# Kernel optimization log

Measured on AMD Instinct MI355X. Metric: run time of the kernel, lower is better.

The kernel has to match this reference:

```python
import jax, jax.numpy as jnp
import numpy as np
from itertools import product

D = 96  # input grid resolution; after subdivision it is 2*D = 192
N_VOX = 20000
C_IN = 64
C_OUT = 64

OFFSETS = jnp.array(list(product([-1, 0, 1], repeat=3)), dtype=jnp.int32)   # [27,3] conv neighborhood
CHILD = jnp.array(list(product([0, 1], repeat=3)), dtype=jnp.int32)        # [8,3] subdivision children


def _lin(coords, d):
    # linearize (z,y,x)-style coords into a flat index for the dense lookup grid
    return (coords[:, 0] * d + coords[:, 1]) * d + coords[:, 2]


def _submanifold_conv3d(coords, feats, W, b, d):
    """Submanifold sparse 3x3x3 conv: output only at active sites.
    coords: [N,3] int32, feats: [N,Cin], W: [27,Cin,Cout], b: [Cout]."""
    n = coords.shape[0]
    grid = jnp.full((d * d * d,), -1, dtype=jnp.int32).at[_lin(coords, d)].set(
        jnp.arange(n, dtype=jnp.int32))
    out = jnp.broadcast_to(b, (n, b.shape[0])).astype(feats.dtype)
    for k in range(27):  # fixed small kernel loop (unrolled under jit)
        nb = coords + OFFSETS[k]
        inb = jnp.all((nb >= 0) & (nb < d), axis=1)
        idx = grid[_lin(jnp.clip(nb, 0, d - 1), d)]
        mask = (inb & (idx >= 0)).astype(feats.dtype)
        f = feats[jnp.maximum(idx, 0)] * mask[:, None]  # gather active neighbors
        out = out + f @ W[k]
    return out


def setup_inputs() -> dict:
    rng = np.random.default_rng(0)
    lin = rng.choice(D ** 3, size=N_VOX, replace=False)  # unique active voxels
    coords = np.stack([lin // (D * D), (lin // D) % D, lin % D], axis=1).astype(np.int32)
    key = jax.random.key(0)
    k1, k2, k3, k4, k5 = jax.random.split(key, 5)
    scale = 1.0 / np.sqrt(27.0 * C_IN)
    return {
        "coords": jnp.asarray(coords),
        "feats": jax.random.normal(k1, (N_VOX, C_IN), jnp.float32),
        "W1": jax.random.normal(k2, (27, C_IN, C_OUT), jnp.float32) * scale,
        "b1": jax.random.normal(k3, (C_OUT,), jnp.float32) * 0.01,
        "W2": jax.random.normal(k4, (27, C_OUT, C_OUT), jnp.float32) * scale,
        "b2": jax.random.normal(k5, (C_OUT,), jnp.float32) * 0.01,
    }


def reference(coords, feats, W1, b1, W2, b2):
    # act_layers: SparseConv3d + SiLU
    h = jax.nn.silu(_submanifold_conv3d(coords, feats, W1, b1, D))
    n = coords.shape[0]
    coords2 = ((coords * 2)[:, None, :] + CHILD[None, :, :]).reshape(8 * n, 3)
    h2 = jnp.repeat(h, 8, axis=0)  # matches (N,8,C)->(8N,C) child order
    # out_layers: SparseConv3d + SiLU at doubled resolution
    return jax.nn.silu(_submanifold_conv3d(coords2, h2, W2, b2, 2 * D))
```

## Files before the change

### kernel.cpp

```cpp
#include <hip/hip_runtime.h>

#define D1 96
#define GRID_VOX (D1 * D1 * D1)
#define CAP1 32
#define CAP2S 8

typedef __attribute__((ext_vector_type(8))) short short8_t;
typedef __attribute__((ext_vector_type(4))) float f32x4;

__device__ __forceinline__ unsigned short bf16rne(float x) {
    unsigned u = __float_as_uint(x);
    return (unsigned short)((u + 0x7FFF + ((u >> 16) & 1)) >> 16);
}
__device__ __forceinline__ void split2(float v, unsigned short& hi,
                                       unsigned short& lo) {
    hi = bf16rne(v);
    float hf = __uint_as_float((unsigned)hi << 16);
    lo = bf16rne(v - hf);
}

__global__ void setup_kernel(const float* __restrict__ W1,
                             const float* __restrict__ W2,
                             int4* __restrict__ grid16,
                             unsigned short* __restrict__ Wpk1h,
                             unsigned short* __restrict__ Wpk1l,
                             unsigned short* __restrict__ Wpk2h,
                             unsigned short* __restrict__ Wpk2l,
                             float* __restrict__ W2e) {
    int b = blockIdx.x;
    if (b < 432) {
        grid16[b * 256 + threadIdx.x] = make_int4(0, 0, 0, 0);
        return;
    }
    int t = (b - 432) * 256 + threadIdx.x;
    if (t < 512) {
        int fid = t >> 6, l = t & 63;
        int kb = fid >> 2, c = fid & 3;
#pragma unroll
        for (int e = 0; e < 8; ++e) {
            int ci = kb * 32 + ((l >> 4) << 3) + e;
            int co = c * 16 + (l & 15);
            unsigned short hi, lo;
            split2(W1[13 * 4096 + ci * 64 + co], hi, lo);
            Wpk1h[(size_t)t * 8 + e] = hi;
            Wpk1l[(size_t)t * 8 + e] = lo;
        }
    } else if (t < 512 + 4096) {
        int u = t - 512;
        int fid = u >> 6, l = u & 63;
        int s = fid >> 3, kb = (fid >> 2) & 1, c = fid & 3;
        int s0 = (s >> 2) & 1, s1 = (s >> 1) & 1, s2 = s & 1;
#pragma unroll
        for (int e = 0; e < 8; ++e) {
            int ci = kb * 32 + ((l >> 4) << 3) + e;
            int co = c * 16 + (l & 15);
            float sum = 0.f;
            for (int o0 = -s0; o0 <= 1 - s0; ++o0)
                for (int o1 = -s1; o1 <= 1 - s1; ++o1)
                    for (int o2 = -s2; o2 <= 1 - s2; ++o2) {
                        int k = (o0 + 1) * 9 + (o1 + 1) * 3 + (o2 + 1);
                        sum += W2[k * 4096 + ci * 64 + co];
                    }
            unsigned short hi, lo;
            split2(sum, hi, lo);
            Wpk2h[(size_t)u * 8 + e] = hi;
            Wpk2l[(size_t)u * 8 + e] = lo;
        }
    } else {
        int r = t - 4608;
        if (r >= 64 * 4096) return;
        int sd = r >> 12, e = r & 4095;
        int s = sd >> 3, d = sd & 7;
        int sa[3] = { (s >> 2) & 1, (s >> 1) & 1, s & 1 };
        int da[3] = { (d >> 2) & 1, (d >> 1) & 1, d & 1 };
        int lo_[3], hi_[3];
        for (int a = 0; a < 3; ++a) {
            int p = sa[a] - 1 + da[a];
            int l = 2 * p - sa[a];     if (l < -1) l = -1;
            int h = 2 * p + 1 - sa[a]; if (h > 1) h = 1;
            lo_[a] = l; hi_[a] = h;
        }
        float sum = 0.f;
        for (int o0 = lo_[0]; o0 <= hi_[0]; ++o0)
            for (int o1 = lo_[1]; o1 <= hi_[1]; ++o1)
                for (int o2 = lo_[2]; o2 <= hi_[2]; ++o2) {
                    int k = (o0 + 1) * 9 + (o1 + 1) * 3 + (o2 + 1);
                    sum += W2[k * 4096 + e];
                }
        W2e[(size_t)sd * 4096 + e] = sum;
    }
}

__global__ void scatter_grid_kernel(const int* __restrict__ coords,
                                    unsigned short* __restrict__ grid, int n) {
    int i = blockIdx.x * blockDim.x + threadIdx.x;
    if (i < n)
        grid[(coords[3 * i] * D1 + coords[3 * i + 1]) * D1 + coords[3 * i + 2]] =
            (unsigned short)(i + 1);
}

__global__ void build_pairs_kernel(const int* __restrict__ coords,
                                   const unsigned short* __restrict__ grid,
                                   int* __restrict__ c1, int* __restrict__ p1,
                                   int* __restrict__ c2s, int* __restrict__ p2s,
                                   int n) {
    int i = blockIdx.x * blockDim.x + threadIdx.x;
    if (i >= n) return;
    int c0 = coords[3 * i], cc1 = coords[3 * i + 1], cc2 = coords[3 * i + 2];

    int jv[27];
#pragma unroll
    for (int k = 0; k < 27; ++k) {
        int o0 = k / 9 - 1, o1 = (k / 3) % 3 - 1, o2 = k % 3 - 1;
        int x0 = c0 + o0, x1 = cc1 + o1, x2 = cc2 + o2;
        bool inb = (unsigned)x0 < D1 && (unsigned)x1 < D1 && (unsigned)x2 < D1;
        jv[k] = inb ? (int)grid[(x0 * D1 + x1) * D1 + x2] - 1 : -1;
    }

    int n1 = 0;
    int n2[8] = {0, 0, 0, 0, 0, 0, 0, 0};
#pragma unroll
    for (int k = 0; k < 27; ++k) {
        if (k == 13) continue;
        int j = jv[k];
        if (j < 0) continue;
        int o0 = k / 9 - 1, o1 = (k / 3) % 3 - 1, o2 = k % 3 - 1;
        p1[(size_t)i * CAP1 + n1] = j | (k << 17);
        ++n1;
#pragma unroll
        for (int s = 0; s < 8; ++s) {
            int d0 = o0 + 1 - ((s >> 2) & 1);
            int d1 = o1 + 1 - ((s >> 1) & 1);
            int d2 = o2 + 1 - (s & 1);
            if (((d0 | d1 | d2) & ~1) == 0) {
                int d = (d0 << 2) | (d1 << 1) | d2;
                p2s[((size_t)i * 8 + s) * CAP2S + n2[s]] = j | (d << 17);
                ++n2[s];
            }
        }
    }
    c1[i] = n1;
#pragma unroll
    for (int s = 0; s < 8; ++s) c2s[i * 8 + s] = n2[s];
}

__device__ __forceinline__ void load_split_A(const float* __restrict__ src,
                                             int arow, int lane, short8_t& ah0,
                                             short8_t& al0, short8_t& ah1,
                                             short8_t& al1) {
    const float* ap = src + (size_t)arow * 64 + ((lane >> 4) << 3);
    f32x4 a0 = *(const f32x4*)(ap);
    f32x4 a1 = *(const f32x4*)(ap + 4);
    f32x4 a2 = *(const f32x4*)(ap + 32);
    f32x4 a3 = *(const f32x4*)(ap + 36);
#pragma unroll
    for (int e = 0; e < 4; ++e) {
        unsigned short hh, ll;
        split2(a0[e], hh, ll); ah0[e] = (short)hh; al0[e] = (short)ll;
        split2(a1[e], hh, ll); ah0[4 + e] = (short)hh; al0[4 + e] = (short)ll;
        split2(a2[e], hh, ll); ah1[e] = (short)hh; al1[e] = (short)ll;
        split2(a3[e], hh, ll); ah1[4 + e] = (short)hh; al1[4 + e] = (short)ll;
    }
}

__device__ __forceinline__ void dense_mfma(const short8_t ah0, const short8_t al0,
                                           const short8_t ah1, const short8_t al1,
                                           const short8_t* __restrict__ Bh,
                                           const short8_t* __restrict__ Bl,
                                           const float* __restrict__ bias,
                                           float* __restrict__ oT, int w,
                                           int lane) {
#pragma unroll 1
    for (int c = 0; c < 4; ++c) {
        short8_t bh0 = Bh[c * 64 + lane];
        short8_t bl0 = Bl[c * 64 + lane];
        short8_t bh1 = Bh[(4 + c) * 64 + lane];
        short8_t bl1 = Bl[(4 + c) * 64 + lane];
        f32x4 acc = {0.f, 0.f, 0.f, 0.f};
        acc = __builtin_amdgcn_mfma_f32_16x16x32_bf16(ah0, bh0, acc, 0, 0, 0);
        acc = __builtin_amdgcn_mfma_f32_16x16x32_bf16(al0, bh0, acc, 0, 0, 0);
        acc = __builtin_amdgcn_mfma_f32_16x16x32_bf16(ah0, bl0, acc, 0, 0, 0);
        acc = __builtin_amdgcn_mfma_f32_16x16x32_bf16(ah1, bh1, acc, 0, 0, 0);
        acc = __builtin_amdgcn_mfma_f32_16x16x32_bf16(al1, bh1, acc, 0, 0, 0);
        acc = __builtin_amdgcn_mfma_f32_16x16x32_bf16(ah1, bl1, acc, 0, 0, 0);
        int col = c * 16 + (lane & 15);
        float bb = bias[col];
#pragma unroll
        for (int r = 0; r < 4; ++r) {
            int row = w * 16 + ((lane >> 4) << 2) + r;
            oT[row * 64 + col] = acc[r] + bb;
        }
    }
}

__device__ __forceinline__ void fixup_pair_lds(const float* __restrict__ fj,
                                               const float* __restrict__ wk,
                                               float* __restrict__ oT, int row,
                                               int lane) {
    float a0 = 0.f, a1 = 0.f, a2 = 0.f, a3 = 0.f;
#pragma unroll
    for (int c4 = 0; c4 < 16; ++c4) {
        f32x4 fv = *(const f32x4*)(fj + c4 * 4);
        a0 += fv[0] * wk[(c4 * 4 + 0) * 64 + lane];
        a1 += fv[1] * wk[(c4 * 4 + 1) * 64 + lane];
        a2 += fv[2] * wk[(c4 * 4 + 2) * 64 + lane];
        a3 += fv[3] * wk[(c4 * 4 + 3) * 64 + lane];
    }
    atomicAdd(&oT[row * 64 + lane], (a0 + a1) + (a2 + a3));
}

__device__ __forceinline__ void scan64(int cnt, int lane, int* pfxs, int* cnts,
                                       int* nps) {
    int val = cnt;
#pragma unroll
    for (int off = 1; off < 64; off <<= 1) {
        int v2 = __shfl_up(val, off);
        if (lane >= off) val += v2;
    }
    pfxs[lane] = val - cnt;
    cnts[lane] = cnt;
    if (lane == 63) nps[0] = val;
}

__global__ __launch_bounds__(256) void conv1_fused_kernel(
    const float* __restrict__ feats, const float* __restrict__ W1,
    const unsigned short* __restrict__ Wpk1h,
    const unsigned short* __restrict__ Wpk1l, const float* __restrict__ b1,
    const int* __restrict__ c1, const int* __restrict__ p1,
    float* __restrict__ h, int n) {
    __shared__ __align__(16) float oT[4096];
    __shared__ __align__(16) float fstage[64 * 64];
    __shared__ int pl[2048];
    __shared__ int pfxs[64], cnts_s[64], nps[1];
    int base = blockIdx.x * 64;
    int t = threadIdx.x, w = t >> 6, lane = t & 63;

    if (t < 64) {
        int cnt = (base + lane < n) ? c1[base + lane] : 0;
        scan64(cnt, lane, pfxs, cnts_s, nps);
    }

    int arow = base + w * 16 + (lane & 15);
    if (arow >= n) arow = n - 1;
    short8_t ah0, al0, ah1, al1;
    load_split_A(feats, arow, lane, ah0, al0, ah1, al1);
    dense_mfma(ah0, al0, ah1, al1, (const short8_t*)Wpk1h,
               (const short8_t*)Wpk1l, b1, oT, w, lane);
    __syncthreads();

    {
        int row = t & 63, e0 = t >> 6;
        int cr = cnts_s[row], pf = pfxs[row];
        for (int e = e0; e < cr; e += 4)
            pl[pf + e] = p1[(size_t)(base + row) * CAP1 + e] | (row << 23);
    }
    __syncthreads();

    int np = nps[0];
    for (int cb = 0; cb < np; cb += 64) {
        {
            int p = cb + (t >> 2), qq = t & 3;
            if (p < np) {
                int j = pl[p] & 0x1FFFF;
                const f32x4* src = (const f32x4*)(feats + (size_t)j * 64 + qq * 16);
                f32x4* dst = (f32x4*)&fstage[(p - cb) * 64 + qq * 16];
#pragma unroll
                for (int q = 0; q < 4; ++q) dst[q] = src[q];
            }
        }
        __syncthreads();
        int pe = np < cb + 64 ? np : cb + 64;
#pragma unroll 1
        for (int p = cb + w; p < pe; p += 4) {
            int se = pl[p];
            int k = (se >> 17) & 31, row = (se >> 23) & 63;
            fixup_pair_lds(&fstage[(p - cb) * 64], W1 + (size_t)k * 4096, oT,
                           row, lane);
        }
        __syncthreads();
    }

    {
        int r = t >> 2, q0 = (t & 3) * 16;
        if (base + r < n) {
#pragma unroll
            for (int jj = 0; jj < 4; ++jj) {
                f32x4 v = *(f32x4*)&oT[r * 64 + q0 + jj * 4];
#pragma unroll
                for (int u = 0; u < 4; ++u) v[u] = v[u] / (1.f + __expf(-v[u]));
                *(f32x4*)&h[(size_t)(base + r) * 64 + q0 + jj * 4] = v;
            }
        }
    }
}

__global__ __launch_bounds__(256) void conv2_fused_kernel(
    const float* __restrict__ h, const unsigned short* __restrict__ Wpk2h,
    const unsigned short* __restrict__ Wpk2l, const float* __restrict__ W2e,
    const float* __restrict__ b2, const int* __restrict__ c2s,
    const int* __restrict__ p2s, float* __restrict__ out, int n) {
    __shared__ __align__(16) float oT[4096];
    __shared__ __align__(16) float fstage[32 * 64];
    __shared__ int pl[512];
    __shared__ int pfxs[64], cnts_s[64], nps[1];
    int base = blockIdx.x * 64, s = blockIdx.y;
    int t = threadIdx.x, w = t >> 6, lane = t & 63;

    if (t < 64) {
        int cnt = (base + lane < n) ? c2s[(size_t)(base + lane) * 8 + s] : 0;
        scan64(cnt, lane, pfxs, cnts_s, nps);
    }

    int arow = base + w * 16 + (lane & 15);
    if (arow >= n) arow = n - 1;
    short8_t ah0, al0, ah1, al1;
    load_split_A(h, arow, lane, ah0, al0, ah1, al1);
    dense_mfma(ah0, al0, ah1, al1,
               (const short8_t*)Wpk2h + (size_t)s * 8 * 64,
               (const short8_t*)Wpk2l + (size_t)s * 8 * 64, b2, oT, w, lane);
    __syncthreads();

    {
        int row = t & 63, e0 = t >> 6;
        int cr = cnts_s[row], pf = pfxs[row];
        for (int e = e0; e < cr; e += 4)
            pl[pf + e] =
                p2s[((size_t)(base + row) * 8 + s) * CAP2S + e] | (row << 23);
    }
    __syncthreads();

    int np = nps[0];
    for (int cb = 0; cb < np; cb += 32) {
        {
            int p = cb + (t >> 3), qq = t & 7;
            if (p < np) {
                int j = pl[p] & 0x1FFFF;
                const f32x4* src = (const f32x4*)(h + (size_t)j * 64 + qq * 8);
                f32x4* dst = (f32x4*)&fstage[(p - cb) * 64 + qq * 8];
                dst[0] = src[0];
                dst[1] = src[1];
            }
        }
        __syncthreads();
        int pe = np < cb + 32 ? np : cb + 32;
#pragma unroll 1
        for (int p = cb + w; p < pe; p += 4) {
            int se = pl[p];
            int d = (se >> 17) & 31, row = (se >> 23) & 63;
            fixup_pair_lds(&fstage[(p - cb) * 64],
                           W2e + (size_t)(s * 8 + d) * 4096, oT, row, lane);
        }
        __syncthreads();
    }

    {
        int r = t >> 2, q0 = (t & 3) * 16;
        if (base + r < n) {
#pragma unroll
            for (int jj = 0; jj < 4; ++jj) {
                f32x4 v = *(f32x4*)&oT[r * 64 + q0 + jj * 4];
#pragma unroll
                for (int u = 0; u < 4; ++u) v[u] = v[u] / (1.f + __expf(-v[u]));
                *(f32x4*)&out[((size_t)(base + r) * 8 + s) * 64 + q0 + jj * 4] = v;
            }
        }
    }
}

extern "C" void kernel_launch(void* const* d_in, const int* in_sizes, int n_in,
                              void* d_out, int out_size, void* d_ws,
                              size_t ws_size, hipStream_t stream) {
    const int* coords = (const int*)d_in[0];
    const float* feats = (const float*)d_in[1];
    const float* W1 = (const float*)d_in[2];
    const float* b1 = (const float*)d_in[3];
    const float* W2 = (const float*)d_in[4];
    const float* b2 = (const float*)d_in[5];
    float* out = (float*)d_out;

    int n = in_sizes[0] / 3;
    int nblk = (n + 63) / 64;

    char* ws = (char*)d_ws;
    size_t off = 0;
    auto alloc = [&](size_t bytes) {
        size_t o = off;
        off = (off + bytes + 255) & ~(size_t)255;
        return o;
    };
    unsigned short* grid1 = (unsigned short*)(ws + alloc((size_t)GRID_VOX * 2));
    float* h      = (float*)(ws + alloc((size_t)n * 64 * 4));
    float* W2e    = (float*)(ws + alloc(64 * 4096 * 4));
    unsigned short* Wpk1h = (unsigned short*)(ws + alloc(512 * 8 * 2));
    unsigned short* Wpk1l = (unsigned short*)(ws + alloc(512 * 8 * 2));
    unsigned short* Wpk2h = (unsigned short*)(ws + alloc(4096 * 8 * 2));
    unsigned short* Wpk2l = (unsigned short*)(ws + alloc(4096 * 8 * 2));
    int*   c1     = (int*)(ws + alloc((size_t)n * 9 * 4));
    int*   c2s    = c1 + n;
    int*   p1     = (int*)(ws + alloc((size_t)n * CAP1 * 4));
    int*   p2s    = (int*)(ws + alloc((size_t)n * 8 * CAP2S * 4));

    setup_kernel<<<1474, 256, 0, stream>>>(W1, W2, (int4*)grid1, Wpk1h, Wpk1l,
                                           Wpk2h, Wpk2l, W2e);
    scatter_grid_kernel<<<(n + 255) / 256, 256, 0, stream>>>(coords, grid1, n);
    build_pairs_kernel<<<(n + 255) / 256, 256, 0, stream>>>(
        coords, grid1, c1, p1, c2s, p2s, n);

    conv1_fused_kernel<<<nblk, 256, 0, stream>>>(feats, W1, Wpk1h, Wpk1l, b1,
                                                 c1, p1, h, n);
    conv2_fused_kernel<<<dim3(nblk, 8), 256, 0, stream>>>(
        h, Wpk2h, Wpk2l, W2e, b2, c2s, p2s, out, n);
}
```

Baseline: 88.18 us.

## Split conv2 into sparse fixup kernel and dense MFMA kernel

Replaces the fused conv2 kernel (one block per 64 rows per subdivision child, with LDS staging of neighbor pairs) with two kernels. A per-voxel wave kernel first computes cross-parent neighbor contributions directly into out, skipping voxels with no pairs. A 512-thread dense MFMA kernel then handles all 8 children per block with the A fragments shared in LDS, adding bias, any fixup partial and SiLU. This removes the redundant per-s reloading of h and the LDS pair staging, at the cost of an extra launch and a read-modify-write of out.

```diff
diff --git a/kernel.cpp b/kernel.cpp
--- a/kernel.cpp
+++ b/kernel.cpp
@@ -17,6 +17,9 @@
     hi = bf16rne(v);
     float hf = __uint_as_float((unsigned)hi << 16);
     lo = bf16rne(v - hf);
+}
+__device__ __forceinline__ float silu(float v) {
+    return v / (1.f + __expf(-v));
 }
 
 __global__ void setup_kernel(const float* __restrict__ W1,
@@ -287,81 +290,136 @@
             for (int jj = 0; jj < 4; ++jj) {
                 f32x4 v = *(f32x4*)&oT[r * 64 + q0 + jj * 4];
 #pragma unroll
-                for (int u = 0; u < 4; ++u) v[u] = v[u] / (1.f + __expf(-v[u]));
+                for (int u = 0; u < 4; ++u) v[u] = silu(v[u]);
                 *(f32x4*)&h[(size_t)(base + r) * 64 + q0 + jj * 4] = v;
             }
         }
     }
 }
 
-__global__ __launch_bounds__(256) void conv2_fused_kernel(
+__global__ __launch_bounds__(256) void conv2_fix_kernel(
+    const float* __restrict__ h, const float* __restrict__ W2e,
+    const int* __restrict__ c2s, const int* __restrict__ p2s,
+    float* __restrict__ out, int n) {
+    int w = threadIdx.x >> 6, lane = threadIdx.x & 63;
+    int i = blockIdx.x * 4 + w;
+    if (i >= n) return;
+    int cnt8 = (lane < 8) ? c2s[(size_t)i * 8 + lane] : 0;
+    if (__ballot(cnt8 > 0) == 0ULL) return;
+
+#pragma unroll 1
+    for (int s = 0; s < 8; ++s) {
+        int cl = __shfl(cnt8, s);
+        if (cl == 0) continue;
+        float tot = 0.f;
+#pragma unroll 1
+        for (int e = 0; e < cl; ++e) {
+            int se = __builtin_amdgcn_readfirstlane(
+                p2s[((size_t)i * 8 + s) * CAP2S + e]);
+            int j = se & 0x1FFFF, d = (se >> 17) & 7;
+            const float* fj = h + (size_t)j * 64;
+            const float* wk = W2e + (size_t)(s * 8 + d) * 4096;
+            float a0 = 0.f, a1 = 0.f, a2 = 0.f, a3 = 0.f;
+#pragma unroll
+            for (int c4 = 0; c4 < 16; ++c4) {
+                f32x4 fv = *(const f32x4*)(fj + c4 * 4);
+                a0 += fv[0] * wk[(c4 * 4 + 0) * 64 + lane];
+                a1 += fv[1] * wk[(c4 * 4 + 1) * 64 + lane];
+                a2 += fv[2] * wk[(c4 * 4 + 2) * 64 + lane];
+                a3 += fv[3] * wk[(c4 * 4 + 3) * 64 + lane];
+            }
+            tot += (a0 + a1) + (a2 + a3);
+        }
+        out[((size_t)i * 8 + s) * 64 + lane] = tot;
+    }
+}
+
+__global__ __launch_bounds__(512) void conv2_dense_kernel(
     const float* __restrict__ h, const unsigned short* __restrict__ Wpk2h,
-    const unsigned short* __restrict__ Wpk2l, const float* __restrict__ W2e,
-    const float* __restrict__ b2, const int* __restrict__ c2s,
-    const int* __restrict__ p2s, float* __restrict__ out, int n) {
-    __shared__ __align__(16) float oT[4096];
-    __shared__ __align__(16) float fstage[32 * 64];
-    __shared__ int pl[512];
-    __shared__ int pfxs[64], cnts_s[64], nps[1];
-    int base = blockIdx.x * 64, s = blockIdx.y;
-    int t = threadIdx.x, w = t >> 6, lane = t & 63;
-
-    if (t < 64) {
-        int cnt = (base + lane < n) ? c2s[(size_t)(base + lane) * 8 + s] : 0;
-        scan64(cnt, lane, pfxs, cnts_s, nps);
-    }
-
-    int arow = base + w * 16 + (lane & 15);
-    if (arow >= n) arow = n - 1;
-    short8_t ah0, al0, ah1, al1;
-    load_split_A(h, arow, lane, ah0, al0, ah1, al1);
-    dense_mfma(ah0, al0, ah1, al1,
-               (const short8_t*)Wpk2h + (size_t)s * 8 * 64,
-               (const short8_t*)Wpk2l + (size_t)s * 8 * 64, b2, oT, w, lane);
+    const unsigned short* __restrict__ Wpk2l, const float* __restrict__ b2,
+    const int* __restrict__ c2s, float* __restrict__ out, int n) {
+    __shared__ short8_t afrag[2][4][2][64];
+    int base = blockIdx.x * 64;
+    int t = threadIdx.x, lane = t & 63, u = t >> 6;
+
+    {
+        int tr = u >> 1, kb = u & 1;
+        int gr = base + tr * 16 + (lane & 15);
+        if (gr >= n) gr = n - 1;
+        const float* ap = h + (size_t)gr * 64 + kb * 32 + ((lane >> 4) << 3);
+        f32x4 a0 = *(const f32x4*)ap;
+        f32x4 a1 = *(const f32x4*)(ap + 4);
+        short8_t hi, lo;
+#pragma unroll
+        for (int e = 0; e < 4; ++e) {
+            unsigned short hh, ll;
+            split2(a0[e], hh, ll); hi[e] = (short)hh; lo[e] = (short)ll;
+            split2(a1[e], hh, ll); hi[4 + e] = (short)hh; lo[4 + e] = (short)ll;
+        }
+        afrag[0][tr][kb][lane] = hi;
+        afrag[1][tr][kb][lane] = lo;
+    }
     __syncthreads();
 
-    {
-        int row = t & 63, e0 = t >> 6;
-        int cr = cnts_s[row], pf = pfxs[row];
-        for (int e = e0; e < cr; e += 4)
-            pl[pf + e] =
-                p2s[((size_t)(base + row) * 8 + s) * CAP2S + e] | (row << 23);
-    }
-    __syncthreads();
-
-    int np = nps[0];
-    for (int cb = 0; cb < np; cb += 32) {
-        {
-            int p = cb + (t >> 3), qq = t & 7;
-            if (p < np) {
-                int j = pl[p] & 0x1FFFF;
-                const f32x4* src = (const f32x4*)(h + (size_t)j * 64 + qq * 8);
-                f32x4* dst = (f32x4*)&fstage[(p - cb) * 64 + qq * 8];
-                dst[0] = src[0];
-                dst[1] = src[1];
-            }
-        }
-        __syncthreads();
-        int pe = np < cb + 32 ? np : cb + 32;
-#pragma unroll 1
-        for (int p = cb + w; p < pe; p += 4) {
-            int se = pl[p];
-            int d = (se >> 17) & 31, row = (se >> 23) & 63;
-            fixup_pair_lds(&fstage[(p - cb) * 64],
-                           W2e + (size_t)(s * 8 + d) * 4096, oT, row, lane);
-        }
-        __syncthreads();
-    }
-
-    {
-        int r = t >> 2, q0 = (t & 3) * 16;
-        if (base + r < n) {
-#pragma unroll
-            for (int jj = 0; jj < 4; ++jj) {
-                f32x4 v = *(f32x4*)&oT[r * 64 + q0 + jj * 4];
-#pragma unroll
-                for (int u = 0; u < 4; ++u) v[u] = v[u] / (1.f + __expf(-v[u]));
-                *(f32x4*)&out[((size_t)(base + r) * 8 + s) * 64 + q0 + jj * 4] = v;
+    int s = u;
+    int ci = base + lane; if (ci >= n) ci = n - 1;
+    bool flag = (base + lane < n) && (c2s[(size_t)ci * 8 + s] > 0);
+    unsigned long long pmask = __ballot(flag);
+
+    const short8_t* Bh = (const short8_t*)Wpk2h;
+    const short8_t* Bl = (const short8_t*)Wpk2l;
+    short8_t bh[4][2], bl[4][2];
+#pragma unroll
+    for (int tc = 0; tc < 4; ++tc)
+#pragma unroll
+        for (int kb = 0; kb < 2; ++kb) {
+            bh[tc][kb] = Bh[(size_t)(((s * 2 + kb) * 4 + tc)) * 64 + lane];
+            bl[tc][kb] = Bl[(size_t)(((s * 2 + kb) * 4 + tc)) * 64 + lane];
+        }
+
+    f32x4 acc[4][4];
+#pragma unroll
+    for (int a = 0; a < 4; ++a)
+#pragma unroll
+        for (int b = 0; b < 4; ++b) acc[a][b] = (f32x4){0.f, 0.f, 0.f, 0.f};
+
+#pragma unroll
+    for (int tr = 0; tr < 4; ++tr) {
+        short8_t ah0 = afrag[0][tr][0][lane];
+        short8_t al0 = afrag[1][tr][0][lane];
+        short8_t ah1 = afrag[0][tr][1][lane];
+        short8_t al1 = afrag[1][tr][1][lane];
+#pragma unroll
+        for (int tc = 0; tc < 4; ++tc) {
+            f32x4 a = acc[tr][tc];
+            a = __builtin_amdgcn_mfma_f32_16x16x32_bf16(ah0, bh[tc][0], a, 0, 0, 0);
+            a = __builtin_amdgcn_mfma_f32_16x16x32_bf16(al0, bh[tc][0], a, 0, 0, 0);
+            a = __builtin_amdgcn_mfma_f32_16x16x32_bf16(ah0, bl[tc][0], a, 0, 0, 0);
+            a = __builtin_amdgcn_mfma_f32_16x16x32_bf16(ah1, bh[tc][1], a, 0, 0, 0);
+            a = __builtin_amdgcn_mfma_f32_16x16x32_bf16(al1, bh[tc][1], a, 0, 0, 0);
+            a = __builtin_amdgcn_mfma_f32_16x16x32_bf16(ah1, bl[tc][1], a, 0, 0, 0);
+            acc[tr][tc] = a;
+        }
+    }
+
+    float bb[4];
+#pragma unroll
+    for (int tc = 0; tc < 4; ++tc) bb[tc] = b2[tc * 16 + (lane & 15)];
+
+#pragma unroll
+    for (int tr = 0; tr < 4; ++tr) {
+#pragma unroll
+        for (int r4 = 0; r4 < 4; ++r4) {
+            int R = tr * 16 + ((lane >> 4) << 2) + r4;
+            bool valid = (base + R) < n;
+            bool hasp = valid && ((pmask >> R) & 1ULL);
+            size_t orow = ((size_t)(base + R) * 8 + s) * 64;
+#pragma unroll
+            for (int tc = 0; tc < 4; ++tc) {
+                float v = acc[tr][tc][r4] + bb[tc];
+                if (hasp) v += out[orow + tc * 16 + (lane & 15)];
+                v = silu(v);
+                if (valid) out[orow + tc * 16 + (lane & 15)] = v;
             }
         }
     }
@@ -408,6 +466,7 @@
 
     conv1_fused_kernel<<<nblk, 256, 0, stream>>>(feats, W1, Wpk1h, Wpk1l, b1,
                                                  c1, p1, h, n);
-    conv2_fused_kernel<<<dim3(nblk, 8), 256, 0, stream>>>(
-        h, Wpk2h, Wpk2l, W2e, b2, c2s, p2s, out, n);
-}
+    conv2_fix_kernel<<<(n + 3) / 4, 256, 0, stream>>>(h, W2e, c2s, p2s, out, n);
+    conv2_dense_kernel<<<nblk, 512, 0, stream>>>(h, Wpk2h, Wpk2l, b2, c2s, out,
+                                                 n);
+}
```

Measured after the change: 107.1 us. +21.4%, slower.

## Bin neighbor pairs by kernel offset and keep weight slice in registers

Applied to the files above, without the earlier changes.

Sorts each block's neighbor pair list into bins by kernel offset with an LDS counting sort. Each wave then handles whole bins, loading the 64-entry weight column for that offset into registers once. Neighbor features are read straight from global memory, one float per lane with the next one prefetched, and broadcast by shuffle, which replaces LDS staging of features and per-pair weight reads from global. The risks are load imbalance across the 4 waves, since bins are assigned round-robin, extra register pressure from the 64 weights, and smaller pair-list capacity (1664 and 448 instead of 2048 and 512).

```diff
diff --git a/kernel.cpp b/kernel.cpp
--- a/kernel.cpp
+++ b/kernel.cpp
@@ -17,6 +17,9 @@
     hi = bf16rne(v);
     float hf = __uint_as_float((unsigned)hi << 16);
     lo = bf16rne(v - hf);
+}
+__device__ __forceinline__ float silu(float v) {
+    return v / (1.f + __expf(-v));
 }
 
 __global__ void setup_kernel(const float* __restrict__ W1,
@@ -193,22 +196,6 @@
     }
 }
 
-__device__ __forceinline__ void fixup_pair_lds(const float* __restrict__ fj,
-                                               const float* __restrict__ wk,
-                                               float* __restrict__ oT, int row,
-                                               int lane) {
-    float a0 = 0.f, a1 = 0.f, a2 = 0.f, a3 = 0.f;
-#pragma unroll
-    for (int c4 = 0; c4 < 16; ++c4) {
-        f32x4 fv = *(const f32x4*)(fj + c4 * 4);
-        a0 += fv[0] * wk[(c4 * 4 + 0) * 64 + lane];
-        a1 += fv[1] * wk[(c4 * 4 + 1) * 64 + lane];
-        a2 += fv[2] * wk[(c4 * 4 + 2) * 64 + lane];
-        a3 += fv[3] * wk[(c4 * 4 + 3) * 64 + lane];
-    }
-    atomicAdd(&oT[row * 64 + lane], (a0 + a1) + (a2 + a3));
-}
-
 __device__ __forceinline__ void scan64(int cnt, int lane, int* pfxs, int* cnts,
                                        int* nps) {
     int val = cnt;
@@ -220,6 +207,40 @@
     pfxs[lane] = val - cnt;
     cnts[lane] = cnt;
     if (lane == 63) nps[0] = val;
+}
+
+__device__ __forceinline__ void bin_fixups(const float* __restrict__ src,
+                                           const float* __restrict__ wk,
+                                           const int* __restrict__ pls, int s0,
+                                           int s1, float* __restrict__ oT,
+                                           int lane) {
+    float wreg[64];
+#pragma unroll
+    for (int ci = 0; ci < 64; ++ci) wreg[ci] = wk[ci * 64 + lane];
+
+    int e = pls[s0];
+    float fv = src[(size_t)(e & 0x1FFFF) * 64 + lane];
+#pragma unroll 1
+    for (int p = s0; p < s1; ++p) {
+        int en = 0;
+        float fvn = 0.f;
+        if (p + 1 < s1) {
+            en = pls[p + 1];
+            fvn = src[(size_t)(en & 0x1FFFF) * 64 + lane];
+        }
+        int row = (e >> 23) & 63;
+        float a0 = 0.f, a1 = 0.f, a2 = 0.f, a3 = 0.f;
+#pragma unroll
+        for (int ci = 0; ci < 64; ci += 4) {
+            a0 += __shfl(fv, ci + 0) * wreg[ci + 0];
+            a1 += __shfl(fv, ci + 1) * wreg[ci + 1];
+            a2 += __shfl(fv, ci + 2) * wreg[ci + 2];
+            a3 += __shfl(fv, ci + 3) * wreg[ci + 3];
+        }
+        atomicAdd(&oT[row * 64 + lane], (a0 + a1) + (a2 + a3));
+        e = en;
+        fv = fvn;
+    }
 }
 
 __global__ __launch_bounds__(256) void conv1_fused_kernel(
@@ -229,9 +250,9 @@
     const int* __restrict__ c1, const int* __restrict__ p1,
     float* __restrict__ h, int n) {
     __shared__ __align__(16) float oT[4096];
-    __shared__ __align__(16) float fstage[64 * 64];
-    __shared__ int pl[2048];
+    __shared__ int pl[1664], pls[1664];
     __shared__ int pfxs[64], cnts_s[64], nps[1];
+    __shared__ int binStart[29], binCur[28];
     int base = blockIdx.x * 64;
     int t = threadIdx.x, w = t >> 6, lane = t & 63;
 
@@ -239,6 +260,7 @@
         int cnt = (base + lane < n) ? c1[base + lane] : 0;
         scan64(cnt, lane, pfxs, cnts_s, nps);
     }
+    if (t >= 64 && t < 92) binCur[t - 64] = 0;
 
     int arow = base + w * 16 + (lane & 15);
     if (arow >= n) arow = n - 1;
@@ -257,28 +279,33 @@
     __syncthreads();
 
     int np = nps[0];
-    for (int cb = 0; cb < np; cb += 64) {
-        {
-            int p = cb + (t >> 2), qq = t & 3;
-            if (p < np) {
-                int j = pl[p] & 0x1FFFF;
-                const f32x4* src = (const f32x4*)(feats + (size_t)j * 64 + qq * 16);
-                f32x4* dst = (f32x4*)&fstage[(p - cb) * 64 + qq * 16];
-#pragma unroll
-                for (int q = 0; q < 4; ++q) dst[q] = src[q];
-            }
-        }
-        __syncthreads();
-        int pe = np < cb + 64 ? np : cb + 64;
+    for (int p = t; p < np; p += 256) atomicAdd(&binCur[(pl[p] >> 17) & 31], 1);
+    __syncthreads();
+    if (t == 0) {
+        int acc = 0;
+        for (int b = 0; b < 28; ++b) {
+            binStart[b] = acc;
+            acc += binCur[b];
+        }
+        binStart[28] = acc;
+    }
+    __syncthreads();
+    if (t < 28) binCur[t] = binStart[t];
+    __syncthreads();
+    for (int p = t; p < np; p += 256) {
+        int e = pl[p];
+        int dst = atomicAdd(&binCur[(e >> 17) & 31], 1);
+        pls[dst] = e;
+    }
+    __syncthreads();
+
 #pragma unroll 1
-        for (int p = cb + w; p < pe; p += 4) {
-            int se = pl[p];
-            int k = (se >> 17) & 31, row = (se >> 23) & 63;
-            fixup_pair_lds(&fstage[(p - cb) * 64], W1 + (size_t)k * 4096, oT,
-                           row, lane);
-        }
-        __syncthreads();
-    }
+    for (int b = w; b < 28; b += 4) {
+        int s0 = binStart[b], s1 = binStart[b + 1];
+        if (s0 == s1) continue;
+        bin_fixups(feats, W1 + (size_t)b * 4096, pls, s0, s1, oT, lane);
+    }
+    __syncthreads();
 
     {
         int r = t >> 2, q0 = (t & 3) * 16;
@@ -287,7 +314,7 @@
             for (int jj = 0; jj < 4; ++jj) {
                 f32x4 v = *(f32x4*)&oT[r * 64 + q0 + jj * 4];
 #pragma unroll
-                for (int u = 0; u < 4; ++u) v[u] = v[u] / (1.f + __expf(-v[u]));
+                for (int u = 0; u < 4; ++u) v[u] = silu(v[u]);
                 *(f32x4*)&h[(size_t)(base + r) * 64 + q0 + jj * 4] = v;
             }
         }
@@ -300,9 +327,9 @@
     const float* __restrict__ b2, const int* __restrict__ c2s,
     const int* __restrict__ p2s, float* __restrict__ out, int n) {
     __shared__ __align__(16) float oT[4096];
-    __shared__ __align__(16) float fstage[32 * 64];
-    __shared__ int pl[512];
+    __shared__ int pl[448], pls[448];
     __shared__ int pfxs[64], cnts_s[64], nps[1];
+    __shared__ int binStart[9], binCur[8];
     int base = blockIdx.x * 64, s = blockIdx.y;
     int t = threadIdx.x, w = t >> 6, lane = t & 63;
 
@@ -310,6 +337,7 @@
         int cnt = (base + lane < n) ? c2s[(size_t)(base + lane) * 8 + s] : 0;
         scan64(cnt, lane, pfxs, cnts_s, nps);
     }
+    if (t >= 64 && t < 72) binCur[t - 64] = 0;
 
     int arow = base + w * 16 + (lane & 15);
     if (arow >= n) arow = n - 1;
@@ -330,28 +358,33 @@
     __syncthreads();
 
     int np = nps[0];
-    for (int cb = 0; cb < np; cb += 32) {
-        {
-            int p = cb + (t >> 3), qq = t & 7;
-            if (p < np) {
-                int j = pl[p] & 0x1FFFF;
-                const f32x4* src = (const f32x4*)(h + (size_t)j * 64 + qq * 8);
-                f32x4* dst = (f32x4*)&fstage[(p - cb) * 64 + qq * 8];
-                dst[0] = src[0];
-                dst[1] = src[1];
-            }
-        }
-        __syncthreads();
-        int pe = np < cb + 32 ? np : cb + 32;
+    for (int p = t; p < np; p += 256) atomicAdd(&binCur[(pl[p] >> 17) & 7], 1);
+    __syncthreads();
+    if (t == 0) {
+        int acc = 0;
+        for (int b = 0; b < 8; ++b) {
+            binStart[b] = acc;
+            acc += binCur[b];
+        }
+        binStart[8] = acc;
+    }
+    __syncthreads();
+    if (t < 8) binCur[t] = binStart[t];
+    __syncthreads();
+    for (int p = t; p < np; p += 256) {
+        int e = pl[p];
+        int dst = atomicAdd(&binCur[(e >> 17) & 7], 1);
+        pls[dst] = e;
+    }
+    __syncthreads();
+
 #pragma unroll 1
-        for (int p = cb + w; p < pe; p += 4) {
-            int se = pl[p];
-            int d = (se >> 17) & 31, row = (se >> 23) & 63;
-            fixup_pair_lds(&fstage[(p - cb) * 64],
-                           W2e + (size_t)(s * 8 + d) * 4096, oT, row, lane);
-        }
-        __syncthreads();
-    }
+    for (int b = w; b < 8; b += 4) {
+        int s0 = binStart[b], s1 = binStart[b + 1];
+        if (s0 == s1) continue;
+        bin_fixups(h, W2e + (size_t)(s * 8 + b) * 4096, pls, s0, s1, oT, lane);
+    }
+    __syncthreads();
 
     {
         int r = t >> 2, q0 = (t & 3) * 16;
@@ -360,7 +393,7 @@
             for (int jj = 0; jj < 4; ++jj) {
                 f32x4 v = *(f32x4*)&oT[r * 64 + q0 + jj * 4];
 #pragma unroll
-                for (int u = 0; u < 4; ++u) v[u] = v[u] / (1.f + __expf(-v[u]));
+                for (int u = 0; u < 4; ++u) v[u] = silu(v[u]);
                 *(f32x4*)&out[((size_t)(base + r) * 8 + s) * 64 + q0 + jj * 4] = v;
             }
         }
```

Result: slower. 117.2 us (+32.9%).

## Replace block-synchronized gather staging with per-wave double-buffered neighbor feature fetch

Applied to the files above, without the earlier changes.

The block-wide staging loop, which copied chunks of neighbor feature rows into shared memory between __syncthreads barriers, is replaced by a per-wavefront loop. Each wave loads its own neighbor row (one float per lane) into a small double-buffered LDS slot and computes the fixup dot products right away. This removes the block barriers and the large staging buffers, which should lower LDS use and may raise occupancy. In exchange, each gather is now a serial per-wave load with no block-level batching, so global latency may be exposed. It also relies on wave-synchronous LDS ordering with no explicit barrier between the write and the read.

```diff
diff --git a/kernel.cpp b/kernel.cpp
--- a/kernel.cpp
+++ b/kernel.cpp
@@ -17,6 +17,9 @@
     hi = bf16rne(v);
     float hf = __uint_as_float((unsigned)hi << 16);
     lo = bf16rne(v - hf);
+}
+__device__ __forceinline__ float silu(float v) {
+    return v / (1.f + __expf(-v));
 }
 
 __global__ void setup_kernel(const float* __restrict__ W1,
@@ -193,22 +196,6 @@
     }
 }
 
-__device__ __forceinline__ void fixup_pair_lds(const float* __restrict__ fj,
-                                               const float* __restrict__ wk,
-                                               float* __restrict__ oT, int row,
-                                               int lane) {
-    float a0 = 0.f, a1 = 0.f, a2 = 0.f, a3 = 0.f;
-#pragma unroll
-    for (int c4 = 0; c4 < 16; ++c4) {
-        f32x4 fv = *(const f32x4*)(fj + c4 * 4);
-        a0 += fv[0] * wk[(c4 * 4 + 0) * 64 + lane];
-        a1 += fv[1] * wk[(c4 * 4 + 1) * 64 + lane];
-        a2 += fv[2] * wk[(c4 * 4 + 2) * 64 + lane];
-        a3 += fv[3] * wk[(c4 * 4 + 3) * 64 + lane];
-    }
-    atomicAdd(&oT[row * 64 + lane], (a0 + a1) + (a2 + a3));
-}
-
 __device__ __forceinline__ void scan64(int cnt, int lane, int* pfxs, int* cnts,
                                        int* nps) {
     int val = cnt;
@@ -220,6 +207,34 @@
     pfxs[lane] = val - cnt;
     cnts[lane] = cnt;
     if (lane == 63) nps[0] = val;
+}
+
+__device__ __forceinline__ void fixup_loop(const float* __restrict__ src,
+                                           const float* __restrict__ Wbase,
+                                           const int* __restrict__ pl, int np,
+                                           float fsc[4][2][64],
+                                           float* __restrict__ oT, int w,
+                                           int lane) {
+    int it = 0;
+#pragma unroll 1
+    for (int p = w; p < np; p += 4, ++it) {
+        int e = pl[p];
+        int j = e & 0x1FFFF, tag = (e >> 17) & 31, row = (e >> 23) & 63;
+        float fv = src[(size_t)j * 64 + lane];
+        int buf = it & 1;
+        fsc[w][buf][lane] = fv;
+        const float* wk = Wbase + (size_t)tag * 4096;
+        float a0 = 0.f, a1 = 0.f, a2 = 0.f, a3 = 0.f;
+#pragma unroll
+        for (int c4 = 0; c4 < 16; ++c4) {
+            f32x4 fb = *(f32x4*)&fsc[w][buf][c4 * 4];
+            a0 += fb[0] * wk[(c4 * 4 + 0) * 64 + lane];
+            a1 += fb[1] * wk[(c4 * 4 + 1) * 64 + lane];
+            a2 += fb[2] * wk[(c4 * 4 + 2) * 64 + lane];
+            a3 += fb[3] * wk[(c4 * 4 + 3) * 64 + lane];
+        }
+        atomicAdd(&oT[row * 64 + lane], (a0 + a1) + (a2 + a3));
+    }
 }
 
 __global__ __launch_bounds__(256) void conv1_fused_kernel(
@@ -229,8 +244,8 @@
     const int* __restrict__ c1, const int* __restrict__ p1,
     float* __restrict__ h, int n) {
     __shared__ __align__(16) float oT[4096];
-    __shared__ __align__(16) float fstage[64 * 64];
-    __shared__ int pl[2048];
+    __shared__ __align__(16) float fsc[4][2][64];
+    __shared__ int pl[1664];
     __shared__ int pfxs[64], cnts_s[64], nps[1];
     int base = blockIdx.x * 64;
     int t = threadIdx.x, w = t >> 6, lane = t & 63;
@@ -256,29 +271,8 @@
     }
     __syncthreads();
 
-    int np = nps[0];
-    for (int cb = 0; cb < np; cb += 64) {
-        {
-            int p = cb + (t >> 2), qq = t & 3;
-            if (p < np) {
-                int j = pl[p] & 0x1FFFF;
-                const f32x4* src = (const f32x4*)(feats + (size_t)j * 64 + qq * 16);
-                f32x4* dst = (f32x4*)&fstage[(p - cb) * 64 + qq * 16];
-#pragma unroll
-                for (int q = 0; q < 4; ++q) dst[q] = src[q];
-            }
-        }
-        __syncthreads();
-        int pe = np < cb + 64 ? np : cb + 64;
-#pragma unroll 1
-        for (int p = cb + w; p < pe; p += 4) {
-            int se = pl[p];
-            int k = (se >> 17) & 31, row = (se >> 23) & 63;
-            fixup_pair_lds(&fstage[(p - cb) * 64], W1 + (size_t)k * 4096, oT,
-                           row, lane);
-        }
-        __syncthreads();
-    }
+    fixup_loop(feats, W1, pl, nps[0], fsc, oT, w, lane);
+    __syncthreads();
 
     {
         int r = t >> 2, q0 = (t & 3) * 16;
@@ -287,7 +281,7 @@
             for (int jj = 0; jj < 4; ++jj) {
                 f32x4 v = *(f32x4*)&oT[r * 64 + q0 + jj * 4];
 #pragma unroll
-                for (int u = 0; u < 4; ++u) v[u] = v[u] / (1.f + __expf(-v[u]));
+                for (int u = 0; u < 4; ++u) v[u] = silu(v[u]);
                 *(f32x4*)&h[(size_t)(base + r) * 64 + q0 + jj * 4] = v;
             }
         }
@@ -300,8 +294,8 @@
     const float* __restrict__ b2, const int* __restrict__ c2s,
     const int* __restrict__ p2s, float* __restrict__ out, int n) {
     __shared__ __align__(16) float oT[4096];
-    __shared__ __align__(16) float fstage[32 * 64];
-    __shared__ int pl[512];
+    __shared__ __align__(16) float fsc[4][2][64];
+    __shared__ int pl[448];
     __shared__ int pfxs[64], cnts_s[64], nps[1];
     int base = blockIdx.x * 64, s = blockIdx.y;
     int t = threadIdx.x, w = t >> 6, lane = t & 63;
@@ -329,29 +323,8 @@
     }
     __syncthreads();
 
-    int np = nps[0];
-    for (int cb = 0; cb < np; cb += 32) {
-        {
-            int p = cb + (t >> 3), qq = t & 7;
-            if (p < np) {
-                int j = pl[p] & 0x1FFFF;
-                const f32x4* src = (const f32x4*)(h + (size_t)j * 64 + qq * 8);
-                f32x4* dst = (f32x4*)&fstage[(p - cb) * 64 + qq * 8];
-                dst[0] = src[0];
-                dst[1] = src[1];
-            }
-        }
-        __syncthreads();
-        int pe = np < cb + 32 ? np : cb + 32;
-#pragma unroll 1
-        for (int p = cb + w; p < pe; p += 4) {
-            int se = pl[p];
-            int d = (se >> 17) & 31, row = (se >> 23) & 63;
-            fixup_pair_lds(&fstage[(p - cb) * 64],
-                           W2e + (size_t)(s * 8 + d) * 4096, oT, row, lane);
-        }
-        __syncthreads();
-    }
+    fixup_loop(h, W2e + (size_t)s * 8 * 4096, pl, nps[0], fsc, oT, w, lane);
+    __syncthreads();
 
     {
         int r = t >> 2, q0 = (t & 3) * 16;
@@ -360,7 +333,7 @@
             for (int jj = 0; jj < 4; ++jj) {
                 f32x4 v = *(f32x4*)&oT[r * 64 + q0 + jj * 4];
 #pragma unroll
-                for (int u = 0; u < 4; ++u) v[u] = v[u] / (1.f + __expf(-v[u]));
+                for (int u = 0; u < 4; ++u) v[u] = silu(v[u]);
                 *(f32x4*)&out[((size_t)(base + r) * 8 + s) * 64 + q0 + jj * 4] = v;
             }
         }
```

New measurement: 86.22 us. -2.2%, faster.
